# Optimization experiments

Measured on AMD Instinct MI355X. Metric: run time of the kernel, lower is better.

## Reference

```python
import jax, jax.numpy as jnp
from jax import lax
import numpy as np

EPS = 1e-12  # torch F.normalize eps


def setup_inputs() -> dict:
    key = jax.random.key(0)
    ks = jax.random.split(key, 5)
    B, C, H, W = 8, 192, 128, 128
    heads = 4
    x = jax.random.normal(ks[0], (B, C, H, W), dtype=jnp.float32)
    qkv_w = jax.random.normal(ks[1], (3 * C, C), dtype=jnp.float32) * (1.0 / np.sqrt(C))
    dw_w = jax.random.normal(ks[2], (3 * C, 1, 3, 3), dtype=jnp.float32) * (1.0 / 3.0)
    proj_w = jax.random.normal(ks[3], (C, C), dtype=jnp.float32) * (1.0 / np.sqrt(C))
    temperature = jnp.ones((1, heads, 1, 1), dtype=jnp.float32)
    return {"x": x, "qkv_w": qkv_w, "dw_w": dw_w, "proj_w": proj_w,
            "temperature": temperature, "num_heads": heads}


def _l2_normalize(t):
    # matches torch F.normalize(dim=-1): x / max(||x||, eps)
    n = jnp.sqrt(jnp.sum(t * t, axis=-1, keepdims=True))
    return t / jnp.maximum(n, EPS)


def reference(x, qkv_w, dw_w, proj_w, temperature, num_heads):
    b, c, h, w = x.shape
    # 1x1 conv (no bias) == channel GEMM
    qkv = jnp.einsum('oc,bchw->bohw', qkv_w, x)
    # 3x3 depthwise conv, padding=1, groups=3c
    qkv = lax.conv_general_dilated(
        qkv, dw_w, window_strides=(1, 1), padding='SAME',
        feature_group_count=3 * c,
        dimension_numbers=('NCHW', 'OIHW', 'NCHW'))
    q, k, v = jnp.split(qkv, 3, axis=1)
    hw = h * w
    dh = c // num_heads  # per-head channel dim
    q = q.reshape(b, num_heads, dh, hw)
    k = k.reshape(b, num_heads, dh, hw)
    v = v.reshape(b, num_heads, dh, hw)
    q = _l2_normalize(q)
    k = _l2_normalize(k)
    # channel attention: [b, heads, dh, dh]
    attn = jnp.einsum('bhcn,bhdn->bhcd', q, k) * temperature
    attn = jax.nn.softmax(attn, axis=-1)
    out = jnp.einsum('bhcd,bhdn->bhcn', attn, v).reshape(b, c, h, w)
    out = jnp.einsum('oc,bchw->bohw', proj_w, out)
    return out
```

## Files before the change

kernel.cpp:

```cpp
#include <hip/hip_runtime.h>
#include <hip/hip_bf16.h>

#define CIN 192
#define C3 576
#define HWPX 16384
#define NHEADS 4
#define DH 48

typedef unsigned short ushort_t;
typedef __attribute__((ext_vector_type(8))) short bf16x8;
typedef __attribute__((ext_vector_type(4))) float f32x4;

__device__ __forceinline__ float bf2f(unsigned short u) {
    return __uint_as_float(((unsigned int)u) << 16);
}
__device__ __forceinline__ unsigned short f2bf(float f) {
    unsigned int u = __float_as_uint(f);
    unsigned int r = (u >> 16) & 1u;
    u += 0x7fffu + r;
    return (unsigned short)(u >> 16);
}
__device__ __forceinline__ void up8(uint4 a, float* o) {
    o[0] = __uint_as_float(a.x << 16); o[1] = __uint_as_float(a.x & 0xffff0000u);
    o[2] = __uint_as_float(a.y << 16); o[3] = __uint_as_float(a.y & 0xffff0000u);
    o[4] = __uint_as_float(a.z << 16); o[5] = __uint_as_float(a.z & 0xffff0000u);
    o[6] = __uint_as_float(a.w << 16); o[7] = __uint_as_float(a.w & 0xffff0000u);
}

#define ASYNC_COPY16(gptr, lptr)                                                   \
    __builtin_amdgcn_global_load_lds(                                              \
        (__attribute__((address_space(1))) void*)(gptr),                           \
        (__attribute__((address_space(3))) void*)(lptr), 16, 0, 0)

__global__ __launch_bounds__(256) void k_cvtw(const float* __restrict__ w,
                                              ushort_t* __restrict__ wb) {
    int i = (blockIdx.x * 256 + threadIdx.x) * 4;
    float4 v = *(const float4*)(w + i);
    uint2 pk;
    pk.x = (unsigned)f2bf(v.x) | ((unsigned)f2bf(v.y) << 16);
    pk.y = (unsigned)f2bf(v.z) | ((unsigned)f2bf(v.w) << 16);
    *(uint2*)(wb + i) = pk;
}

__global__ __launch_bounds__(512) void k_gemm(const float* __restrict__ A,
                                              const ushort_t* __restrict__ B,
                                              ushort_t* __restrict__ C) {
    __shared__ ushort_t sA[6 * 128 * 32];
    __shared__ ushort_t sB[2][192 * 32];
    const int t = threadIdx.x;
    const int lane = t & 63, wave = t >> 6;
    const int wrow = wave >> 1, wcol = wave & 1;
    const int pix0 = blockIdx.x * 128;
    const int b = blockIdx.z;

    const int cc = t >> 4;
    const int jj = t & 15;

    {
        float avf[6][8];
#pragma unroll
        for (int c6 = 0; c6 < 6; ++c6) {
            const float* Ab = A + (size_t)b * CIN * HWPX +
                              (size_t)(c6 * 32 + cc) * HWPX + pix0 + jj;
#pragma unroll
            for (int i = 0; i < 8; ++i) avf[c6][i] = Ab[16 * i];
        }
#pragma unroll
        for (int c6 = 0; c6 < 6; ++c6) {
            ushort_t* s = &sA[c6 * 4096];
#pragma unroll
            for (int i = 0; i < 8; ++i) {
                int row = jj + 16 * i;
                int slot = ((cc >> 3) + (row >> 1) + (row >> 3)) & 3;
                s[row * 32 + slot * 8 + (cc & 7)] = f2bf(avf[c6][i]);
            }
        }
    }

    auto stageB = [&](int buf, int og, int kc) {
        const ushort_t* Bb = B + (size_t)og * 192 * CIN;
        {
            int row = t >> 2, slot = t & 3;
            int g = (slot + (row >> 1)) & 3;
            const ushort_t* gp = Bb + (size_t)row * CIN + kc + g * 8;
            ushort_t* lp = &sB[buf][(wave * 64) * 8];
            ASYNC_COPY16(gp, lp);
        }
        if (t < 256) {
            int e = 512 + t;
            int row = e >> 2, slot = e & 3;
            int g = (slot + (row >> 1)) & 3;
            const ushort_t* gp = Bb + (size_t)row * CIN + kc + g * 8;
            ushort_t* lp = &sB[buf][(512 + wave * 64) * 8];
            ASYNC_COPY16(gp, lp);
        }
    };

    f32x4 acc[2][6];
#pragma unroll
    for (int mi = 0; mi < 2; ++mi)
#pragma unroll
        for (int ni = 0; ni < 6; ++ni) acc[mi][ni] = (f32x4){0.f, 0.f, 0.f, 0.f};

    stageB(0, 0, 0);

    const int ocol = lane & 15;
    const int prow = (lane >> 4) * 4;
    const int c = lane >> 4;

#pragma unroll
    for (int og = 0; og < 3; ++og) {
#pragma unroll
        for (int ks = 0; ks < 6; ++ks) {
            const int step = og * 6 + ks;
            const int buf = step & 1;
            __syncthreads();
            if (step + 1 < 18)
                stageB(buf ^ 1, (step + 1) / 6, ((step + 1) % 6) * 32);
            const ushort_t* a_ = &sA[ks * 4096];
            const ushort_t* b_ = sB[buf];
            bf16x8 af[2], bfr[6];
#pragma unroll
            for (int mi = 0; mi < 2; ++mi) {
                int row = wrow * 32 + mi * 16 + (lane & 15);
                int slot = (c + (row >> 1) + (row >> 3)) & 3;
                af[mi] = *(const bf16x8*)&a_[row * 32 + slot * 8];
            }
#pragma unroll
            for (int ni = 0; ni < 6; ++ni) {
                int row = wcol * 96 + ni * 16 + (lane & 15);
                int slot = (c - (row >> 1)) & 3;
                bfr[ni] = *(const bf16x8*)&b_[row * 32 + slot * 8];
            }
#pragma unroll
            for (int mi = 0; mi < 2; ++mi)
#pragma unroll
                for (int ni = 0; ni < 6; ++ni)
                    acc[mi][ni] = __builtin_amdgcn_mfma_f32_16x16x32_bf16(
                        af[mi], bfr[ni], acc[mi][ni], 0, 0, 0);
        }
#pragma unroll
        for (int mi = 0; mi < 2; ++mi) {
            int pix = pix0 + wrow * 32 + mi * 16 + prow;
#pragma unroll
            for (int ni = 0; ni < 6; ++ni) {
                int o = og * 192 + wcol * 96 + ni * 16 + ocol;
                f32x4 v = acc[mi][ni];
                ushort_t* Cp = C + ((size_t)b * C3 + o) * HWPX + pix;
                uint2 pk;
                pk.x = (unsigned)f2bf(v[0]) | ((unsigned)f2bf(v[1]) << 16);
                pk.y = (unsigned)f2bf(v[2]) | ((unsigned)f2bf(v[3]) << 16);
                *(uint2*)Cp = pk;
                acc[mi][ni] = (f32x4){0.f, 0.f, 0.f, 0.f};
            }
        }
    }
}

__global__ __launch_bounds__(256, 1) void k_gramdw(const ushort_t* __restrict__ pre,
                                                   const float* __restrict__ dww,
                                                   float* __restrict__ gpart,
                                                   float* __restrict__ normp) {
    __shared__ char smem[NHEADS * DH * DH * 4];
    ushort_t* sCw = (ushort_t*)smem + (threadIdx.x >> 6) * (96 * 40);
    float* sG = (float*)smem;

    const int chunk = blockIdx.x, h = blockIdx.y, b = blockIdx.z;
    const int t = threadIdx.x;
    const int lane = t & 63, wave = t >> 6;
    const int y0 = chunk * 16;

    const ushort_t* plane[3];
    float wreg[3][9];
    int pxb[3];
#pragma unroll
    for (int u = 0; u < 3; ++u) {
        int id = lane + 64 * u;
        int c96 = id >> 1;
        int gch = (c96 < DH) ? (h * DH + c96) : (CIN + h * DH + (c96 - DH));
        plane[u] = pre + ((size_t)b * C3 + gch) * HWPX;
        pxb[u] = wave * 32 + (id & 1) * 16;
#pragma unroll
        for (int k = 0; k < 9; ++k) wreg[u][k] = dww[gch * 9 + k];
    }

    float ssq[3] = {0.f, 0.f, 0.f};
    f32x4 acc[3][3];
#pragma unroll
    for (int i = 0; i < 3; ++i)
#pragma unroll
        for (int j = 0; j < 3; ++j) acc[i][j] = (f32x4){0.f, 0.f, 0.f, 0.f};

    uint4 ring[3][3][2];
    ushort_t lfr[3][3], rgr[3][3];
    uint4 nx[3][2];
    ushort_t nlf[3], nrg[3];

    auto LOADROW = [&](int YY) {
#pragma unroll
        for (int u = 0; u < 3; ++u) {
            bool ok = ((unsigned)YY < 128u);
            const ushort_t* rp = plane[u] + YY * 128 + pxb[u];
            if (ok) {
                nx[u][0] = *(const uint4*)rp;
                nx[u][1] = *(const uint4*)(rp + 8);
                nlf[u] = (pxb[u] > 0) ? rp[-1] : (ushort_t)0;
                nrg[u] = (pxb[u] + 16 < 128) ? rp[16] : (ushort_t)0;
            } else {
                nx[u][0] = make_uint4(0, 0, 0, 0);
                nx[u][1] = make_uint4(0, 0, 0, 0);
                nlf[u] = 0;
                nrg[u] = 0;
            }
        }
    };
    auto PUT = [&](int rp) {
#pragma unroll
        for (int u = 0; u < 3; ++u) {
            ring[rp][u][0] = nx[u][0];
            ring[rp][u][1] = nx[u][1];
            lfr[rp][u] = nlf[u];
            rgr[rp][u] = nrg[u];
        }
    };

    LOADROW(y0 - 1); PUT(0);
    LOADROW(y0);     PUT(1);
    LOADROW(y0 + 1); PUT(2);

    for (int s = 0; s < 16; ++s) {
        if (s < 15) LOADROW(y0 + s + 2);
#pragma unroll
        for (int u = 0; u < 3; ++u) {
            int id = lane + 64 * u;
            float in[3][18];
#pragma unroll
            for (int r = 0; r < 3; ++r) {
                in[r][0] = bf2f(lfr[r][u]);
                up8(ring[r][u][0], &in[r][1]);
                up8(ring[r][u][1], &in[r][9]);
                in[r][17] = bf2f(rgr[r][u]);
            }
            unsigned pk[8];
#pragma unroll
            for (int j2 = 0; j2 < 8; ++j2) {
                float o0 = 0.f, o1 = 0.f;
#pragma unroll
                for (int ky = 0; ky < 3; ++ky) {
                    o0 = fmaf(wreg[u][ky * 3 + 0], in[ky][2 * j2 + 0], o0);
                    o0 = fmaf(wreg[u][ky * 3 + 1], in[ky][2 * j2 + 1], o0);
                    o0 = fmaf(wreg[u][ky * 3 + 2], in[ky][2 * j2 + 2], o0);
                    o1 = fmaf(wreg[u][ky * 3 + 0], in[ky][2 * j2 + 1], o1);
                    o1 = fmaf(wreg[u][ky * 3 + 1], in[ky][2 * j2 + 2], o1);
                    o1 = fmaf(wreg[u][ky * 3 + 2], in[ky][2 * j2 + 3], o1);
                }
                ssq[u] = fmaf(o0, o0, ssq[u]);
                ssq[u] = fmaf(o1, o1, ssq[u]);
                pk[j2] = (unsigned)f2bf(o0) | ((unsigned)f2bf(o1) << 16);
            }
            uint4* dst = (uint4*)&sCw[(id >> 1) * 40 + ((id & 1) << 4)];
            dst[0] = make_uint4(pk[0], pk[1], pk[2], pk[3]);
            dst[1] = make_uint4(pk[4], pk[5], pk[6], pk[7]);
        }
        {
            bf16x8 af[3], bk[3];
#pragma unroll
            for (int i = 0; i < 3; ++i)
                af[i] = *(const bf16x8*)&sCw[(i * 16 + (lane & 15)) * 40 + (lane >> 4) * 8];
#pragma unroll
            for (int j = 0; j < 3; ++j)
                bk[j] = *(const bf16x8*)&sCw[(48 + j * 16 + (lane & 15)) * 40 + (lane >> 4) * 8];
#pragma unroll
            for (int i = 0; i < 3; ++i)
#pragma unroll
                for (int j = 0; j < 3; ++j)
                    acc[i][j] = __builtin_amdgcn_mfma_f32_16x16x32_bf16(af[i], bk[j],
                                                                        acc[i][j], 0, 0, 0);
        }
        if (s < 15) {
#pragma unroll
            for (int u = 0; u < 3; ++u) {
                ring[0][u][0] = ring[1][u][0]; ring[0][u][1] = ring[1][u][1];
                ring[1][u][0] = ring[2][u][0]; ring[1][u][1] = ring[2][u][1];
                ring[2][u][0] = nx[u][0];      ring[2][u][1] = nx[u][1];
                lfr[0][u] = lfr[1][u]; lfr[1][u] = lfr[2][u]; lfr[2][u] = nlf[u];
                rgr[0][u] = rgr[1][u]; rgr[1][u] = rgr[2][u]; rgr[2][u] = nrg[u];
            }
        }
    }

    __syncthreads();
    const int crow = (lane >> 4) * 4;
    const int dcol = lane & 15;
#pragma unroll
    for (int i = 0; i < 3; ++i)
#pragma unroll
        for (int j = 0; j < 3; ++j)
#pragma unroll
            for (int r = 0; r < 4; ++r)
                sG[(size_t)wave * DH * DH + (i * 16 + crow + r) * DH + j * 16 + dcol] =
                    acc[i][j][r];
    __syncthreads();
    float* g = gpart + (((size_t)(b * NHEADS + h)) * 8 + chunk) * (DH * DH);
    for (int e = t; e < DH * DH; e += 256)
        g[e] = sG[e] + sG[DH * DH + e] + sG[2 * DH * DH + e] + sG[3 * DH * DH + e];

    float* np = normp + ((((size_t)(b * NHEADS + h)) * 8 + chunk) * 4 + wave) * 192;
#pragma unroll
    for (int u = 0; u < 3; ++u) np[lane + 64 * u] = ssq[u];
}

__global__ __launch_bounds__(256) void k_attn(const float* __restrict__ gpart,
                                              const float* __restrict__ normp,
                                              const float* __restrict__ temperature,
                                              float* __restrict__ att) {
    __shared__ float sA[DH][DH + 1];
    __shared__ float nrm[96];
    const int h = blockIdx.x, b = blockIdx.y;
    const int t = threadIdx.x;
    const size_t bh = b * NHEADS + h;
    if (t < 96) {
        float s = 0.f;
        for (int ck = 0; ck < 8; ++ck)
#pragma unroll
            for (int w = 0; w < 4; ++w) {
                const float* np = normp + ((bh * 8 + ck) * 4 + w) * 192 + t * 2;
                s += np[0] + np[1];
            }
        nrm[t] = fmaxf(sqrtf(s), 1e-12f);
    }
    __syncthreads();
    const float* base = gpart + (bh * 8) * (DH * DH);
    for (int e = t; e < DH * DH; e += 256) {
        float s = 0.f;
#pragma unroll
        for (int c8 = 0; c8 < 8; ++c8) s += base[(size_t)c8 * DH * DH + e];
        int c = e / DH, d = e % DH;
        sA[c][d] = s / (nrm[c] * nrm[48 + d]) * temperature[h];
    }
    __syncthreads();
    if (t < DH) {
        float m = -1e30f;
#pragma unroll
        for (int d = 0; d < DH; ++d) m = fmaxf(m, sA[t][d]);
        float s = 0.f;
        float row[DH];
#pragma unroll
        for (int d = 0; d < DH; ++d) {
            row[d] = expf(sA[t][d] - m);
            s += row[d];
        }
        float inv = 1.f / s;
#pragma unroll
        for (int d = 0; d < DH; ++d) sA[t][d] = row[d] * inv;
    }
    __syncthreads();
    float* ob = att + bh * DH * DH;
    for (int e = t; e < DH * DH; e += 256) ob[e] = sA[e / DH][e % DH];
}

__global__ __launch_bounds__(256) void k_mw(const float* __restrict__ att,
                                            const float* __restrict__ proj_w,
                                            ushort_t* __restrict__ Mw) {
    __shared__ float satt[NHEADS][DH][DH];
    __shared__ float sproj[32][CIN];
    const int o0 = blockIdx.x * 32, b = blockIdx.y;
    const int t = threadIdx.x;
    {
        const float4* src = (const float4*)(att + (size_t)b * NHEADS * DH * DH);
        float4* dst = (float4*)&satt[0][0][0];
        for (int e = t; e < NHEADS * DH * DH / 4; e += 256) dst[e] = src[e];
        const float4* ps = (const float4*)(proj_w + (size_t)o0 * CIN);
        float4* pd = (float4*)&sproj[0][0];
        for (int e = t; e < 32 * CIN / 4; e += 256) pd[e] = ps[e];
    }
    __syncthreads();
    ushort_t* ob = Mw + (size_t)b * CIN * CIN;
    for (int e = t; e < 32 * CIN; e += 256) {
        int o = e / CIN, dg = e % CIN;
        int h = dg / DH, d = dg % DH;
        float s = 0.f;
#pragma unroll
        for (int c = 0; c < DH; ++c) s = fmaf(sproj[o][h * DH + c], satt[h][c][d], s);
        int row = o0 + o;
        int ni16 = row >> 4, r = row & 15;
        int ks = dg >> 5, cq = (dg >> 3) & 3, e8 = dg & 7;
        size_t idx = (((size_t)ks * 12 + ni16) * 64 + (cq * 16 + r)) * 8 + e8;
        ob[idx] = f2bf(s);
    }
}

__global__ __launch_bounds__(512) void k_gemmv(const ushort_t* __restrict__ pre,
                                               const float* __restrict__ dww,
                                               const ushort_t* __restrict__ Bp,
                                               float* __restrict__ C) {
    __shared__ ushort_t sA[6 * 128 * 32];
    const int t = threadIdx.x;
    const int lane = t & 63, wave = t >> 6;
    const int wrow = wave >> 1, wcol = wave & 1;
    const int Y = blockIdx.x;
    const int pix0 = Y * 128;
    const int b = blockIdx.z;
    const ushort_t* Bb = Bp + (size_t)b * CIN * CIN;

    const int cc = t >> 4;
    const int jj = t & 15;
    const int x0 = jj * 8;

#pragma unroll
    for (int c6 = 0; c6 < 6; ++c6) {
        int ch = c6 * 32 + cc;
        const ushort_t* pl = pre + ((size_t)b * C3 + 2 * CIN + ch) * HWPX;
        uint4 m[3];
        ushort_t l16[3], rg16[3];
#pragma unroll
        for (int r = 0; r < 3; ++r) {
            int YY = Y - 1 + r;
            bool ok = ((unsigned)YY < 128u);
            const ushort_t* rp = pl + YY * 128;
            if (ok) {
                m[r] = *(const uint4*)(rp + x0);
                l16[r] = (x0 > 0) ? rp[x0 - 1] : (ushort_t)0;
                rg16[r] = (x0 < 120) ? rp[x0 + 8] : (ushort_t)0;
            } else {
                m[r] = make_uint4(0, 0, 0, 0);
                l16[r] = 0;
                rg16[r] = 0;
            }
        }
        float wv[9];
#pragma unroll
        for (int k = 0; k < 9; ++k) wv[k] = dww[(2 * CIN + ch) * 9 + k];
        float in[3][10];
#pragma unroll
        for (int r = 0; r < 3; ++r) {
            in[r][0] = bf2f(l16[r]);
            up8(m[r], &in[r][1]);
            in[r][9] = bf2f(rg16[r]);
        }
        ushort_t* s = &sA[c6 * 4096];
#pragma unroll
        for (int j = 0; j < 8; ++j) {
            float o = 0.f;
#pragma unroll
            for (int ky = 0; ky < 3; ++ky) {
                o = fmaf(wv[ky * 3 + 0], in[ky][j + 0], o);
                o = fmaf(wv[ky * 3 + 1], in[ky][j + 1], o);
                o = fmaf(wv[ky * 3 + 2], in[ky][j + 2], o);
            }
            int row = jj * 8 + j;
            int slot = ((cc >> 3) + (row >> 1) + (row >> 3)) & 3;
            s[row * 32 + slot * 8 + (cc & 7)] = f2bf(o);
        }
    }
    __syncthreads();

    const int c = lane >> 4;
    f32x4 acc[2][6];
#pragma unroll
    for (int mi = 0; mi < 2; ++mi)
#pragma unroll
        for (int ni = 0; ni < 6; ++ni) acc[mi][ni] = (f32x4){0.f, 0.f, 0.f, 0.f};

#pragma unroll
    for (int ks = 0; ks < 6; ++ks) {
        const ushort_t* a_ = &sA[ks * 4096];
        bf16x8 af[2], bfr[6];
#pragma unroll
        for (int mi = 0; mi < 2; ++mi) {
            int row = wrow * 32 + mi * 16 + (lane & 15);
            int slot = (c + (row >> 1) + (row >> 3)) & 3;
            af[mi] = *(const bf16x8*)&a_[row * 32 + slot * 8];
        }
#pragma unroll
        for (int ni = 0; ni < 6; ++ni) {
            size_t fidx = (((size_t)ks * 12 + wcol * 6 + ni) * 64 + lane) * 8;
            bfr[ni] = *(const bf16x8*)&Bb[fidx];
        }
#pragma unroll
        for (int mi = 0; mi < 2; ++mi)
#pragma unroll
            for (int ni = 0; ni < 6; ++ni)
                acc[mi][ni] = __builtin_amdgcn_mfma_f32_16x16x32_bf16(
                    af[mi], bfr[ni], acc[mi][ni], 0, 0, 0);
    }

    const int ocol = lane & 15;
    const int prow = (lane >> 4) * 4;
#pragma unroll
    for (int mi = 0; mi < 2; ++mi) {
        int pix = pix0 + wrow * 32 + mi * 16 + prow;
#pragma unroll
        for (int ni = 0; ni < 6; ++ni) {
            int o = wcol * 96 + ni * 16 + ocol;
            f32x4 v = acc[mi][ni];
            float* Cp = C + ((size_t)b * CIN + o) * HWPX + pix;
            *(float4*)Cp = make_float4(v[0], v[1], v[2], v[3]);
        }
    }
}

extern "C" void kernel_launch(void* const* d_in, const int* in_sizes, int n_in,
                              void* d_out, int out_size, void* d_ws, size_t ws_size,
                              hipStream_t stream) {
    const float* x = (const float*)d_in[0];
    const float* qkv_w = (const float*)d_in[1];
    const float* dw_w = (const float*)d_in[2];
    const float* proj_w = (const float*)d_in[3];
    const float* temperature = (const float*)d_in[4];
    float* out = (float*)d_out;

    char* ws = (char*)d_ws;
    ushort_t* pre = (ushort_t*)ws;
    float* normp = (float*)(ws + 150994944);
    float* gpart = (float*)(ws + 151781376);
    ushort_t* Mw = (ushort_t*)(ws + 154140672);
    float* attb = (float*)(ws + 154730496);
    ushort_t* wq = (ushort_t*)(ws + 155025408);

    k_cvtw<<<dim3(108), 256, 0, stream>>>(qkv_w, wq);
    k_gemm<<<dim3(128, 1, 8), 512, 0, stream>>>(x, wq, pre);
    k_gramdw<<<dim3(8, NHEADS, 8), 256, 0, stream>>>(pre, dw_w, gpart, normp);
    k_attn<<<dim3(NHEADS, 8), 256, 0, stream>>>(gpart, normp, temperature, attb);
    k_mw<<<dim3(6, 8), 256, 0, stream>>>(attb, proj_w, Mw);
    k_gemmv<<<dim3(128, 1, 8), 512, 0, stream>>>(pre, dw_w, Mw, out);
}
```

Measured before the change: 201.9 us.

## Halve QKV GEMM pixel tile and triple-buffer weight staging with one barrier per step

The QKV projection GEMM now uses 64-pixel tiles with 256 threads per block, doubling the grid to 2048 blocks. Weight tiles are triple-buffered and prefetched two steps ahead, and a vmcnt wait plus a single barrier per k-step replaces the __syncthreads before each stage. This aims to raise occupancy and overlap the async global-to-LDS loads with MFMA work. Each block now reloads the weight panels for fewer pixels, so total weight traffic through L2 goes up.

Result: slower. 210.6 us (+4.3%).

```diff
diff --git a/kernel.cpp b/kernel.cpp
--- a/kernel.cpp
+++ b/kernel.cpp
@@ -42,19 +42,19 @@
     *(uint2*)(wb + i) = pk;
 }
 
-__global__ __launch_bounds__(512) void k_gemm(const float* __restrict__ A,
+__global__ __launch_bounds__(256) void k_gemm(const float* __restrict__ A,
                                               const ushort_t* __restrict__ B,
                                               ushort_t* __restrict__ C) {
-    __shared__ ushort_t sA[6 * 128 * 32];
-    __shared__ ushort_t sB[2][192 * 32];
+    __shared__ ushort_t sA[6 * 64 * 32];
+    __shared__ ushort_t sB[3][192 * 32];
     const int t = threadIdx.x;
     const int lane = t & 63, wave = t >> 6;
     const int wrow = wave >> 1, wcol = wave & 1;
-    const int pix0 = blockIdx.x * 128;
+    const int pix0 = blockIdx.x * 64;
     const int b = blockIdx.z;
 
-    const int cc = t >> 4;
-    const int jj = t & 15;
+    const int cc = t >> 3;
+    const int jj = t & 7;
 
     {
         float avf[6][8];
@@ -63,14 +63,14 @@
             const float* Ab = A + (size_t)b * CIN * HWPX +
                               (size_t)(c6 * 32 + cc) * HWPX + pix0 + jj;
 #pragma unroll
-            for (int i = 0; i < 8; ++i) avf[c6][i] = Ab[16 * i];
+            for (int i = 0; i < 8; ++i) avf[c6][i] = Ab[8 * i];
         }
 #pragma unroll
         for (int c6 = 0; c6 < 6; ++c6) {
-            ushort_t* s = &sA[c6 * 4096];
+            ushort_t* s = &sA[c6 * 2048];
 #pragma unroll
             for (int i = 0; i < 8; ++i) {
-                int row = jj + 16 * i;
+                int row = jj + 8 * i;
                 int slot = ((cc >> 3) + (row >> 1) + (row >> 3)) & 3;
                 s[row * 32 + slot * 8 + (cc & 7)] = f2bf(avf[c6][i]);
             }
@@ -79,19 +79,13 @@
 
     auto stageB = [&](int buf, int og, int kc) {
         const ushort_t* Bb = B + (size_t)og * 192 * CIN;
-        {
-            int row = t >> 2, slot = t & 3;
-            int g = (slot + (row >> 1)) & 3;
-            const ushort_t* gp = Bb + (size_t)row * CIN + kc + g * 8;
-            ushort_t* lp = &sB[buf][(wave * 64) * 8];
-            ASYNC_COPY16(gp, lp);
-        }
-        if (t < 256) {
-            int e = 512 + t;
+#pragma unroll
+        for (int r = 0; r < 3; ++r) {
+            int e = r * 256 + t;
             int row = e >> 2, slot = e & 3;
             int g = (slot + (row >> 1)) & 3;
             const ushort_t* gp = Bb + (size_t)row * CIN + kc + g * 8;
-            ushort_t* lp = &sB[buf][(512 + wave * 64) * 8];
+            ushort_t* lp = &sB[buf][(r * 256 + wave * 64) * 8];
             ASYNC_COPY16(gp, lp);
         }
     };
@@ -103,55 +97,58 @@
         for (int ni = 0; ni < 6; ++ni) acc[mi][ni] = (f32x4){0.f, 0.f, 0.f, 0.f};
 
     stageB(0, 0, 0);
-
+    stageB(1, 0, 32);
+    __syncthreads();
+
+    const int c = lane >> 4;
     const int ocol = lane & 15;
     const int prow = (lane >> 4) * 4;
-    const int c = lane >> 4;
-
-#pragma unroll
-    for (int og = 0; og < 3; ++og) {
-#pragma unroll
-        for (int ks = 0; ks < 6; ++ks) {
-            const int step = og * 6 + ks;
-            const int buf = step & 1;
-            __syncthreads();
-            if (step + 1 < 18)
-                stageB(buf ^ 1, (step + 1) / 6, ((step + 1) % 6) * 32);
-            const ushort_t* a_ = &sA[ks * 4096];
-            const ushort_t* b_ = sB[buf];
-            bf16x8 af[2], bfr[6];
+
+#pragma unroll
+    for (int s = 0; s < 18; ++s) {
+        if (s > 0) {
+            asm volatile("s_waitcnt vmcnt(3)" ::: "memory");
+            __builtin_amdgcn_s_barrier();
+        }
+        const ushort_t* a_ = &sA[(s % 6) * 2048];
+        const ushort_t* b_ = sB[s % 3];
+        bf16x8 af[2], bfr[6];
+#pragma unroll
+        for (int mi = 0; mi < 2; ++mi) {
+            int row = wrow * 32 + mi * 16 + (lane & 15);
+            int slot = (c + (row >> 1) + (row >> 3)) & 3;
+            af[mi] = *(const bf16x8*)&a_[row * 32 + slot * 8];
+        }
+#pragma unroll
+        for (int ni = 0; ni < 6; ++ni) {
+            int row = wcol * 96 + ni * 16 + (lane & 15);
+            int slot = (c - (row >> 1)) & 3;
+            bfr[ni] = *(const bf16x8*)&b_[row * 32 + slot * 8];
+        }
+        if (s + 2 < 18)
+            stageB((s + 2) % 3, (s + 2) / 6, ((s + 2) % 6) * 32);
+#pragma unroll
+        for (int mi = 0; mi < 2; ++mi)
+#pragma unroll
+            for (int ni = 0; ni < 6; ++ni)
+                acc[mi][ni] = __builtin_amdgcn_mfma_f32_16x16x32_bf16(
+                    af[mi], bfr[ni], acc[mi][ni], 0, 0, 0);
+        if ((s % 6) == 5) {
+            const int og = s / 6;
 #pragma unroll
             for (int mi = 0; mi < 2; ++mi) {
-                int row = wrow * 32 + mi * 16 + (lane & 15);
-                int slot = (c + (row >> 1) + (row >> 3)) & 3;
-                af[mi] = *(const bf16x8*)&a_[row * 32 + slot * 8];
-            }
-#pragma unroll
-            for (int ni = 0; ni < 6; ++ni) {
-                int row = wcol * 96 + ni * 16 + (lane & 15);
-                int slot = (c - (row >> 1)) & 3;
-                bfr[ni] = *(const bf16x8*)&b_[row * 32 + slot * 8];
-            }
-#pragma unroll
-            for (int mi = 0; mi < 2; ++mi)
-#pragma unroll
-                for (int ni = 0; ni < 6; ++ni)
-                    acc[mi][ni] = __builtin_amdgcn_mfma_f32_16x16x32_bf16(
-                        af[mi], bfr[ni], acc[mi][ni], 0, 0, 0);
-        }
-#pragma unroll
-        for (int mi = 0; mi < 2; ++mi) {
-            int pix = pix0 + wrow * 32 + mi * 16 + prow;
-#pragma unroll
-            for (int ni = 0; ni < 6; ++ni) {
-                int o = og * 192 + wcol * 96 + ni * 16 + ocol;
-                f32x4 v = acc[mi][ni];
-                ushort_t* Cp = C + ((size_t)b * C3 + o) * HWPX + pix;
-                uint2 pk;
-                pk.x = (unsigned)f2bf(v[0]) | ((unsigned)f2bf(v[1]) << 16);
-                pk.y = (unsigned)f2bf(v[2]) | ((unsigned)f2bf(v[3]) << 16);
-                *(uint2*)Cp = pk;
-                acc[mi][ni] = (f32x4){0.f, 0.f, 0.f, 0.f};
+                int pix = pix0 + wrow * 32 + mi * 16 + prow;
+#pragma unroll
+                for (int ni = 0; ni < 6; ++ni) {
+                    int o = og * 192 + wcol * 96 + ni * 16 + ocol;
+                    f32x4 v = acc[mi][ni];
+                    ushort_t* Cp = C + ((size_t)b * C3 + o) * HWPX + pix;
+                    uint2 pk;
+                    pk.x = (unsigned)f2bf(v[0]) | ((unsigned)f2bf(v[1]) << 16);
+                    pk.y = (unsigned)f2bf(v[2]) | ((unsigned)f2bf(v[3]) << 16);
+                    *(uint2*)Cp = pk;
+                    acc[mi][ni] = (f32x4){0.f, 0.f, 0.f, 0.f};
+                }
             }
         }
     }
@@ -519,7 +516,7 @@
     ushort_t* wq = (ushort_t*)(ws + 155025408);
 
     k_cvtw<<<dim3(108), 256, 0, stream>>>(qkv_w, wq);
-    k_gemm<<<dim3(128, 1, 8), 512, 0, stream>>>(x, wq, pre);
+    k_gemm<<<dim3(256, 1, 8), 256, 0, stream>>>(x, wq, pre);
     k_gramdw<<<dim3(8, NHEADS, 8), 256, 0, stream>>>(pre, dw_w, gpart, normp);
     k_attn<<<dim3(NHEADS, 8), 256, 0, stream>>>(gpart, normp, temperature, attb);
     k_mw<<<dim3(6, 8), 256, 0, stream>>>(attb, proj_w, Mw);
```
